# Kernel tuning notes

Measured on AMD Instinct MI355X. Metric: run time of the kernel, lower is better.

## Reference

```python
import jax, jax.numpy as jnp
import numpy as np

K = 5               # kernel size of the causal/dilated convs
N_LAYERS = 30       # params.n_dilation_conv_layers
CYCLE = 10          # n_dilation_conv_layers / n_dilation_cycles
MU = 255.0          # quantization_channels - 1 for mu-law expansion
B, T = 8, 262144


def dil_causal_conv(x, w, b, d):
    """Single-channel dilated causal conv. x:[B,1,T], w:[K], b:scalar/[1]."""
    P = (K - 1) * d
    xp = jnp.pad(x, ((0, 0), (0, 0), (P, 0)))
    Tn = x.shape[-1]
    # cross-correlation, matching torch Conv1d with left pad then right crop
    y = w[0] * xp[..., 0:Tn]
    for j in range(1, K):
        y = y + w[j] * xp[..., j * d: j * d + Tn]
    return y + b


def setup_inputs() -> dict:
    key = jax.random.key(0)
    ks = jax.random.split(key, 14)
    n = lambda k, shape, s=0.2: jax.random.normal(k, shape, dtype=jnp.float32) * s
    return {
        "x": jax.random.normal(ks[0], (B, 1, T), dtype=jnp.float32),
        "causal_w": n(ks[1], (K,)),
        "causal_b": n(ks[2], (1,)),
        "filter_w": n(ks[3], (N_LAYERS, K)),
        "filter_b": n(ks[4], (N_LAYERS,)),
        "gate_w": n(ks[5], (N_LAYERS, K)),
        "gate_b": n(ks[6], (N_LAYERS,)),
        "res_w": n(ks[7], (N_LAYERS,)),
        "res_b": n(ks[8], (N_LAYERS,)),
        "conv1_w": n(ks[9], (1,)),
        "conv1_b": n(ks[10], (1,)),
        "conv2_w": n(ks[11], (1,)),
        "conv2_b": n(ks[12], (1,)),
    }


def reference(x, causal_w, causal_b, filter_w, filter_b, gate_w, gate_b,
              res_w, res_b, conv1_w, conv1_b, conv2_w, conv2_b):
    dilations = [2 ** (k % CYCLE) for k in range(N_LAYERS)]
    h = dil_causal_conv(x, causal_w, causal_b, 1)
    skip = jnp.zeros_like(h)
    for k, d in enumerate(dilations):
        f = jnp.tanh(dil_causal_conv(h, filter_w[k], filter_b[k], d))
        g = jax.nn.sigmoid(dil_causal_conv(h, gate_w[k], gate_b[k], d))
        o = f * g                      # gated activation (skip output)
        h = res_w[k] * o + res_b[k] + h  # 1x1 residual conv + residual add
        skip = skip + o
    out = conv1_w * jax.nn.relu(skip) + conv1_b   # 1x1 conv
    out = conv2_w * jax.nn.relu(out) + conv2_b    # 1x1 conv
    # mu-law expanding, quantization_channels=256
    out = jnp.sign(out) * jnp.expm1(jnp.abs(out) * jnp.log1p(MU)) / MU
    return jax.nn.softmax(out, axis=-1)
```

## Files before the change

kernel.cpp:

```cpp
#include <hip/hip_runtime.h>

#define T_LEN 262144
#define B_SZ 8
#define CHUNK 8192
#define HALO 4096
#define NTHREADS 1024
#define NGROUPW 3
#define NGROUPS ((CHUNK + HALO) / 4)
#define CHUNKS_PER_ROW (T_LEN / CHUNK)
#define NBLOCKS (B_SZ * CHUNKS_PER_ROW)
#define LOG2E 1.4426950408889634f
#define NEG2LOG2E (-2.8853900817779268f)
#define NEGLOG2E  (-1.4426950408889634f)

__device__ __forceinline__ float frcp(float x)  { return __builtin_amdgcn_rcpf(x); }
__device__ __forceinline__ float fexp2(float x) { return __builtin_amdgcn_exp2f(x); }
__device__ __forceinline__ float4 ld4(const float* p) { return *(const float4*)p; }
__device__ __forceinline__ void st4(float* p, float4 v) { *(float4*)p = v; }
__device__ __forceinline__ float4 f4(float v) { return make_float4(v, v, v, v); }
__device__ __forceinline__ float4 fma4(float a, float4 b, float4 c) {
    return make_float4(__builtin_fmaf(a, b.x, c.x), __builtin_fmaf(a, b.y, c.y),
                       __builtin_fmaf(a, b.z, c.z), __builtin_fmaf(a, b.w, c.w));
}
__device__ __forceinline__ float4 add4(float4 a, float4 b) {
    return make_float4(a.x + b.x, a.y + b.y, a.z + b.z, a.w + b.w);
}
__device__ __forceinline__ float gate1(float af, float ag) {
    float E1 = fexp2(af), E2 = fexp2(ag);
    float d1 = 1.0f + E1;
    float den = __builtin_fmaf(E2, d1, d1);
    return (1.0f - E1) * frcp(den);
}
__device__ __forceinline__ float4 resid4(float rwv, float4 o, float4 hw, float rbv) {
    return make_float4(__builtin_fmaf(rwv, o.x, hw.x + rbv), __builtin_fmaf(rwv, o.y, hw.y + rbv),
                       __builtin_fmaf(rwv, o.z, hw.z + rbv), __builtin_fmaf(rwv, o.w, hw.w + rbv));
}
__device__ __forceinline__ float mulaw(float v, float c1wv, float c1bv, float c2wv, float c2bv) {
    float a  = __builtin_fmaf(c1wv, fmaxf(v, 0.0f), c1bv);
    float b2 = __builtin_fmaf(c2wv, fmaxf(a, 0.0f), c2bv);
    float m  = fexp2(fabsf(b2) * 8.0f) - 1.0f;
    return copysignf(m * (1.0f / 255.0f), b2);
}
__device__ __forceinline__ uint2 pk4(float4 v) {
    uint2 u;
    u.x = (__float_as_uint(v.y) & 0xffff0000u) | (__float_as_uint(v.x) >> 16);
    u.y = (__float_as_uint(v.w) & 0xffff0000u) | (__float_as_uint(v.z) >> 16);
    return u;
}
__device__ __forceinline__ float4 up4(uint2 u) {
    return make_float4(__uint_as_float(u.x << 16), __uint_as_float(u.x),
                       __uint_as_float(u.y << 16), __uint_as_float(u.y));
}

template <int STAGE>
__global__ __launch_bounds__(NTHREADS, 4)
void stage_kernel(const float* __restrict__ in,
                  const float* __restrict__ cw, const float* __restrict__ cb,
                  const float* __restrict__ fw, const float* __restrict__ fb,
                  const float* __restrict__ gw, const float* __restrict__ gb,
                  const float* __restrict__ rw, const float* __restrict__ rb,
                  float* __restrict__ hout, float* __restrict__ skio,
                  const float* __restrict__ c1w, const float* __restrict__ c1b,
                  const float* __restrict__ c2w, const float* __restrict__ c2b,
                  float2* __restrict__ blockstats)
{
    __shared__ uint2 bufl[2][NGROUPS];
    __shared__ float red[NTHREADS / 64];

    const int tid = threadIdx.x;
    const int bid = blockIdx.x;
    const int row = bid / CHUNKS_PER_ROW;
    const int chunk = bid % CHUNKS_PER_ROW;
    const int rowbase = row * T_LEN;
    const int base_t = chunk * CHUNK;
    const bool first = (chunk == 0);
    const float* inb = in + rowbase + base_t - HALO;

    float4 h[NGROUPW];
    #pragma unroll
    for (int w = 0; w < NGROUPW; ++w) {
        int G = tid + w * NTHREADS;
        if (w == 0 && first) h[w] = f4(0.0f);
        else                 h[w] = ld4(inb + 4 * G);
        bufl[0][G] = pk4(h[w]);
    }
    float4 sk1, sk2;
    if (STAGE == 0) { sk1 = f4(0.0f); sk2 = f4(0.0f); }
    else {
        sk1 = ld4(skio + rowbase + base_t + 4 * tid);
        sk2 = ld4(skio + rowbase + base_t + 4096 + 4 * tid);
    }
    __syncthreads();

    int c = 0;
    if (STAGE == 0) {
        const float c0 = cw[4], c1 = cw[3], c2 = cw[2], c3 = cw[1], c4 = cw[0];
        const float bb = cb[0];
        #pragma unroll
        for (int w = 0; w < NGROUPW; ++w) {
            int G = tid + w * NTHREADS;
            int gm = G - 1; if (w == 0) gm = gm < 0 ? 0 : gm;
            float4 T = up4(bufl[0][gm]);
            float4 hw = h[w];
            float4 t1 = make_float4(T.w, hw.x, hw.y, hw.z);
            float4 t2 = make_float4(T.z, T.w, hw.x, hw.y);
            float4 t3 = make_float4(T.y, T.z, T.w, hw.x);
            float4 t4 = make_float4(T.x, T.y, T.z, T.w);
            float4 acc = fma4(c0, hw, f4(bb));
            acc = fma4(c1, t1, acc);
            acc = fma4(c2, t2, acc);
            acc = fma4(c3, t3, acc);
            acc = fma4(c4, t4, acc);
            if (w == 0 && first) acc = f4(0.0f);
            h[w] = acc;
            bufl[1][G] = pk4(acc);
        }
        __syncthreads();
        c = 1;
    }

    #pragma unroll
    for (int k = 0; k < 10; ++k) {
        const int d = 1 << k;
        const int L = STAGE * 10 + k;
        const float* fwL = fw + 5 * L;
        const float* gwL = gw + 5 * L;
        const float wf0 = fwL[4] * NEG2LOG2E, wf1 = fwL[3] * NEG2LOG2E,
                    wf2 = fwL[2] * NEG2LOG2E, wf3 = fwL[1] * NEG2LOG2E,
                    wf4 = fwL[0] * NEG2LOG2E;
        const float wg0 = gwL[4] * NEGLOG2E, wg1 = gwL[3] * NEGLOG2E,
                    wg2 = gwL[2] * NEGLOG2E, wg3 = gwL[1] * NEGLOG2E,
                    wg4 = gwL[0] * NEGLOG2E;
        const float fbv = fb[L] * NEG2LOG2E, gbv = gb[L] * NEGLOG2E;
        const float rwv = rw[L], rbv = rb[L];

        #pragma unroll
        for (int w = 0; w < NGROUPW; ++w) {
            const int G = tid + w * NTHREADS;
            float4 hw = h[w];
            float4 t1, t2, t3, t4;
            if (d >= 4) {
                const int DG = d >> 2;
                int g1 = G - DG, g2 = G - 2 * DG, g3 = G - 3 * DG, g4 = G - 4 * DG;
                if (w == 0) {
                    g1 = g1 < 0 ? 0 : g1; g2 = g2 < 0 ? 0 : g2;
                    g3 = g3 < 0 ? 0 : g3; g4 = g4 < 0 ? 0 : g4;
                }
                t1 = up4(bufl[c][g1]);
                t2 = up4(bufl[c][g2]);
                t3 = up4(bufl[c][g3]);
                t4 = up4(bufl[c][g4]);
            } else if (d == 1) {
                int gm = G - 1; if (w == 0) gm = gm < 0 ? 0 : gm;
                float4 T = up4(bufl[c][gm]);
                t1 = make_float4(T.w, hw.x, hw.y, hw.z);
                t2 = make_float4(T.z, T.w, hw.x, hw.y);
                t3 = make_float4(T.y, T.z, T.w, hw.x);
                t4 = make_float4(T.x, T.y, T.z, T.w);
            } else {
                int gm1 = G - 1, gm2 = G - 2;
                if (w == 0) { gm1 = gm1 < 0 ? 0 : gm1; gm2 = gm2 < 0 ? 0 : gm2; }
                float4 T1 = up4(bufl[c][gm1]);
                float4 T2 = up4(bufl[c][gm2]);
                t1 = make_float4(T1.z, T1.w, hw.x, hw.y);
                t2 = T1;
                t3 = make_float4(T2.z, T2.w, T1.x, T1.y);
                t4 = T2;
            }
            float4 af = fma4(wf0, hw, f4(fbv));
            af = fma4(wf1, t1, af); af = fma4(wf2, t2, af);
            af = fma4(wf3, t3, af); af = fma4(wf4, t4, af);
            float4 ag = fma4(wg0, hw, f4(gbv));
            ag = fma4(wg1, t1, ag); ag = fma4(wg2, t2, ag);
            ag = fma4(wg3, t3, ag); ag = fma4(wg4, t4, ag);
            float4 o;
            o.x = gate1(af.x, ag.x);
            o.y = gate1(af.y, ag.y);
            o.z = gate1(af.z, ag.z);
            o.w = gate1(af.w, ag.w);
            float4 nh = resid4(rwv, o, hw, rbv);
            if (w == 0 && first) nh = f4(0.0f);
            h[w] = nh;
            if (k < 9) bufl[c ^ 1][G] = pk4(nh);
            if (w == 1) sk1 = add4(sk1, o);
            if (w == 2) sk2 = add4(sk2, o);
        }
        if (k < 9) __syncthreads();
        c ^= 1;
    }

    if (STAGE < 2) {
        st4(hout + rowbase + base_t + 4 * tid, h[1]);
        st4(hout + rowbase + base_t + 4096 + 4 * tid, h[2]);
        st4(skio + rowbase + base_t + 4 * tid, sk1);
        st4(skio + rowbase + base_t + 4096 + 4 * tid, sk2);
    } else {
        const float c1wv = c1w[0], c1bv = c1b[0], c2wv = c2w[0], c2bv = c2b[0];
        float4 p1, p2;
        p1.x = mulaw(sk1.x, c1wv, c1bv, c2wv, c2bv);
        p1.y = mulaw(sk1.y, c1wv, c1bv, c2wv, c2bv);
        p1.z = mulaw(sk1.z, c1wv, c1bv, c2wv, c2bv);
        p1.w = mulaw(sk1.w, c1wv, c1bv, c2wv, c2bv);
        p2.x = mulaw(sk2.x, c1wv, c1bv, c2wv, c2bv);
        p2.y = mulaw(sk2.y, c1wv, c1bv, c2wv, c2bv);
        p2.z = mulaw(sk2.z, c1wv, c1bv, c2wv, c2bv);
        p2.w = mulaw(sk2.w, c1wv, c1bv, c2wv, c2bv);
        st4(skio + rowbase + base_t + 4 * tid, p1);
        st4(skio + rowbase + base_t + 4096 + 4 * tid, p2);

        float pmax = fmaxf(fmaxf(fmaxf(p1.x, p1.y), fmaxf(p1.z, p1.w)),
                           fmaxf(fmaxf(p2.x, p2.y), fmaxf(p2.z, p2.w)));
        #pragma unroll
        for (int off = 32; off; off >>= 1) pmax = fmaxf(pmax, __shfl_xor(pmax, off, 64));
        if ((tid & 63) == 0) red[tid >> 6] = pmax;
        __syncthreads();
        float bmax = red[0];
        #pragma unroll
        for (int i = 1; i < NTHREADS / 64; ++i) bmax = fmaxf(bmax, red[i]);
        __syncthreads();

        float ps = fexp2((p1.x - bmax) * LOG2E) + fexp2((p1.y - bmax) * LOG2E)
                 + fexp2((p1.z - bmax) * LOG2E) + fexp2((p1.w - bmax) * LOG2E)
                 + fexp2((p2.x - bmax) * LOG2E) + fexp2((p2.y - bmax) * LOG2E)
                 + fexp2((p2.z - bmax) * LOG2E) + fexp2((p2.w - bmax) * LOG2E);
        #pragma unroll
        for (int off = 32; off; off >>= 1) ps += __shfl_xor(ps, off, 64);
        if ((tid & 63) == 0) red[tid >> 6] = ps;
        __syncthreads();
        if (tid == 0) {
            float s = 0.0f;
            #pragma unroll
            for (int i = 0; i < NTHREADS / 64; ++i) s += red[i];
            blockstats[bid] = make_float2(bmax, s);
        }
    }
}

__global__ __launch_bounds__(64)
void combine_kernel(const float2* __restrict__ bs, float2* __restrict__ rs)
{
    const int row = blockIdx.x;
    const int lane = threadIdx.x;
    float bm = -3.0e38f, s = 0.0f;
    if (lane < CHUNKS_PER_ROW) {
        float2 v = bs[row * CHUNKS_PER_ROW + lane];
        bm = v.x; s = v.y;
    }
    float m = bm;
    #pragma unroll
    for (int off = 32; off; off >>= 1) m = fmaxf(m, __shfl_xor(m, off, 64));
    float c = s * fexp2((bm - m) * LOG2E);
    #pragma unroll
    for (int off = 32; off; off >>= 1) c += __shfl_xor(c, off, 64);
    if (lane == 0) rs[row] = make_float2(m, 1.0f / c);
}

__global__ __launch_bounds__(NTHREADS)
void norm_kernel(float* __restrict__ p, const float2* __restrict__ rs)
{
    const int tid = threadIdx.x, bid = blockIdx.x;
    const int row = bid / CHUNKS_PER_ROW;
    const float2 st = rs[row];
    const int base = row * T_LEN + (bid % CHUNKS_PER_ROW) * CHUNK + 4 * tid;
    #pragma unroll
    for (int part = 0; part < 2; ++part) {
        float* q = p + base + part * 4096;
        float4 v = ld4(q);
        v.x = fexp2((v.x - st.x) * LOG2E) * st.y;
        v.y = fexp2((v.y - st.x) * LOG2E) * st.y;
        v.z = fexp2((v.z - st.x) * LOG2E) * st.y;
        v.w = fexp2((v.w - st.x) * LOG2E) * st.y;
        st4(q, v);
    }
}

extern "C" void kernel_launch(void* const* d_in, const int* in_sizes, int n_in,
                              void* d_out, int out_size, void* d_ws, size_t ws_size,
                              hipStream_t stream)
{
    (void)in_sizes; (void)n_in; (void)out_size; (void)ws_size;
    const float* x   = (const float*)d_in[0];
    const float* cw  = (const float*)d_in[1];
    const float* cb  = (const float*)d_in[2];
    const float* fw  = (const float*)d_in[3];
    const float* fb  = (const float*)d_in[4];
    const float* gw  = (const float*)d_in[5];
    const float* gb  = (const float*)d_in[6];
    const float* rw  = (const float*)d_in[7];
    const float* rb  = (const float*)d_in[8];
    const float* c1w = (const float*)d_in[9];
    const float* c1b = (const float*)d_in[10];
    const float* c2w = (const float*)d_in[11];
    const float* c2b = (const float*)d_in[12];
    float* out = (float*)d_out;

    const size_t NTOT = (size_t)B_SZ * T_LEN;
    float*  hA = (float*)d_ws;
    float*  hB = (float*)((char*)d_ws + NTOT * 4);
    float2* bs = (float2*)((char*)d_ws + 2 * NTOT * 4);
    float2* rs = (float2*)((char*)d_ws + 2 * NTOT * 4 + 4096);

    stage_kernel<0><<<NBLOCKS, NTHREADS, 0, stream>>>(x,  cw, cb, fw, fb, gw, gb, rw, rb,
                                                      hA, out, c1w, c1b, c2w, c2b, bs);
    stage_kernel<1><<<NBLOCKS, NTHREADS, 0, stream>>>(hA, cw, cb, fw, fb, gw, gb, rw, rb,
                                                      hB, out, c1w, c1b, c2w, c2b, bs);
    stage_kernel<2><<<NBLOCKS, NTHREADS, 0, stream>>>(hB, cw, cb, fw, fb, gw, gb, rw, rb,
                                                      nullptr, out, c1w, c1b, c2w, c2b, bs);
    combine_kernel<<<B_SZ, 64, 0, stream>>>(bs, rs);
    norm_kernel<<<NBLOCKS, NTHREADS, 0, stream>>>(out, rs);
}
```

Baseline: 85.04 us.

## Halve chunk size, store inter-stage activations as bf16, skip dead halo work

Shrinks each block's output chunk from 8192 to 4096 samples while keeping the 4096-sample halo. Each thread now holds two float4 groups instead of three, and occupancy is raised to 8 blocks per CU. Inter-stage hidden states are written and read as packed bf16 (uint2) to halve that global traffic. Halo positions whose results cannot reach the output are skipped per layer, and those paths drop the clamp logic. The cost is double the blocks, so halo recompute rises relative to useful work, bf16 truncation is added between stages, and the combine kernel now assumes exactly 64 chunks per row.

```diff
diff --git a/kernel.cpp b/kernel.cpp
--- a/kernel.cpp
+++ b/kernel.cpp
@@ -2,10 +2,9 @@
 
 #define T_LEN 262144
 #define B_SZ 8
-#define CHUNK 8192
+#define CHUNK 4096
 #define HALO 4096
 #define NTHREADS 1024
-#define NGROUPW 3
 #define NGROUPS ((CHUNK + HALO) / 4)
 #define CHUNKS_PER_ROW (T_LEN / CHUNK)
 #define NBLOCKS (B_SZ * CHUNKS_PER_ROW)
@@ -13,27 +12,39 @@
 #define NEG2LOG2E (-2.8853900817779268f)
 #define NEGLOG2E  (-1.4426950408889634f)
 
+typedef float f32x4 __attribute__((ext_vector_type(4)));
+
 __device__ __forceinline__ float frcp(float x)  { return __builtin_amdgcn_rcpf(x); }
 __device__ __forceinline__ float fexp2(float x) { return __builtin_amdgcn_exp2f(x); }
-__device__ __forceinline__ float4 ld4(const float* p) { return *(const float4*)p; }
-__device__ __forceinline__ void st4(float* p, float4 v) { *(float4*)p = v; }
-__device__ __forceinline__ float4 f4(float v) { return make_float4(v, v, v, v); }
-__device__ __forceinline__ float4 fma4(float a, float4 b, float4 c) {
-    return make_float4(__builtin_fmaf(a, b.x, c.x), __builtin_fmaf(a, b.y, c.y),
-                       __builtin_fmaf(a, b.z, c.z), __builtin_fmaf(a, b.w, c.w));
-}
-__device__ __forceinline__ float4 add4(float4 a, float4 b) {
-    return make_float4(a.x + b.x, a.y + b.y, a.z + b.z, a.w + b.w);
-}
-__device__ __forceinline__ float gate1(float af, float ag) {
-    float E1 = fexp2(af), E2 = fexp2(ag);
-    float d1 = 1.0f + E1;
-    float den = __builtin_fmaf(E2, d1, d1);
-    return (1.0f - E1) * frcp(den);
-}
-__device__ __forceinline__ float4 resid4(float rwv, float4 o, float4 hw, float rbv) {
-    return make_float4(__builtin_fmaf(rwv, o.x, hw.x + rbv), __builtin_fmaf(rwv, o.y, hw.y + rbv),
-                       __builtin_fmaf(rwv, o.z, hw.z + rbv), __builtin_fmaf(rwv, o.w, hw.w + rbv));
+__device__ __forceinline__ f32x4 splat(float s) { f32x4 r = {s, s, s, s}; return r; }
+__device__ __forceinline__ f32x4 sfma(float s, f32x4 v, f32x4 a) {
+    return __builtin_elementwise_fma(splat(s), v, a);
+}
+__device__ __forceinline__ uint2 pk4(f32x4 v) {
+    uint2 u;
+    u.x = __builtin_amdgcn_perm(__float_as_uint(v.y), __float_as_uint(v.x), 0x07060302u);
+    u.y = __builtin_amdgcn_perm(__float_as_uint(v.w), __float_as_uint(v.z), 0x07060302u);
+    return u;
+}
+__device__ __forceinline__ f32x4 up4(uint2 u) {
+    f32x4 r;
+    r.x = __uint_as_float(u.x << 16);
+    r.y = __uint_as_float(u.x);
+    r.z = __uint_as_float(u.y << 16);
+    r.w = __uint_as_float(u.y);
+    return r;
+}
+__device__ __forceinline__ f32x4 gate4(f32x4 af, f32x4 ag) {
+    f32x4 E1, E2;
+    E1.x = fexp2(af.x); E1.y = fexp2(af.y); E1.z = fexp2(af.z); E1.w = fexp2(af.w);
+    E2.x = fexp2(ag.x); E2.y = fexp2(ag.y); E2.z = fexp2(ag.z); E2.w = fexp2(ag.w);
+    f32x4 d1  = E1 + splat(1.0f);
+    f32x4 den = __builtin_elementwise_fma(E2, d1, d1);
+    f32x4 num = splat(1.0f) - E1;
+    f32x4 r;
+    r.x = num.x * frcp(den.x); r.y = num.y * frcp(den.y);
+    r.z = num.z * frcp(den.z); r.w = num.w * frcp(den.w);
+    return r;
 }
 __device__ __forceinline__ float mulaw(float v, float c1wv, float c1bv, float c2wv, float c2bv) {
     float a  = __builtin_fmaf(c1wv, fmaxf(v, 0.0f), c1bv);
@@ -41,25 +52,15 @@
     float m  = fexp2(fabsf(b2) * 8.0f) - 1.0f;
     return copysignf(m * (1.0f / 255.0f), b2);
 }
-__device__ __forceinline__ uint2 pk4(float4 v) {
-    uint2 u;
-    u.x = (__float_as_uint(v.y) & 0xffff0000u) | (__float_as_uint(v.x) >> 16);
-    u.y = (__float_as_uint(v.w) & 0xffff0000u) | (__float_as_uint(v.z) >> 16);
-    return u;
-}
-__device__ __forceinline__ float4 up4(uint2 u) {
-    return make_float4(__uint_as_float(u.x << 16), __uint_as_float(u.x),
-                       __uint_as_float(u.y << 16), __uint_as_float(u.y));
-}
 
 template <int STAGE>
-__global__ __launch_bounds__(NTHREADS, 4)
-void stage_kernel(const float* __restrict__ in,
+__global__ __launch_bounds__(NTHREADS, 8)
+void stage_kernel(const void* __restrict__ in_,
                   const float* __restrict__ cw, const float* __restrict__ cb,
                   const float* __restrict__ fw, const float* __restrict__ fb,
                   const float* __restrict__ gw, const float* __restrict__ gb,
                   const float* __restrict__ rw, const float* __restrict__ rb,
-                  float* __restrict__ hout, float* __restrict__ skio,
+                  uint2* __restrict__ hout, float* __restrict__ skio,
                   const float* __restrict__ c1w, const float* __restrict__ c1b,
                   const float* __restrict__ c2w, const float* __restrict__ c2b,
                   float2* __restrict__ blockstats)
@@ -74,22 +75,30 @@
     const int rowbase = row * T_LEN;
     const int base_t = chunk * CHUNK;
     const bool first = (chunk == 0);
-    const float* inb = in + rowbase + base_t - HALO;
-
-    float4 h[NGROUPW];
-    #pragma unroll
-    for (int w = 0; w < NGROUPW; ++w) {
-        int G = tid + w * NTHREADS;
-        if (w == 0 && first) h[w] = f4(0.0f);
-        else                 h[w] = ld4(inb + 4 * G);
-        bufl[0][G] = pk4(h[w]);
-    }
-    float4 sk1, sk2;
-    if (STAGE == 0) { sk1 = f4(0.0f); sk2 = f4(0.0f); }
-    else {
-        sk1 = ld4(skio + rowbase + base_t + 4 * tid);
-        sk2 = ld4(skio + rowbase + base_t + 4096 + 4 * tid);
-    }
+
+    f32x4 h[2];
+    if (STAGE == 0) {
+        const float* inb = (const float*)in_ + rowbase + base_t - HALO;
+        #pragma unroll
+        for (int w = 0; w < 2; ++w) {
+            int G = tid + w * NTHREADS;
+            if (w == 0 && first) h[w] = splat(0.0f);
+            else                 h[w] = *(const f32x4*)(inb + 4 * G);
+            bufl[0][G] = pk4(h[w]);
+        }
+    } else {
+        const uint2* inb = (const uint2*)in_ + ((rowbase + base_t - HALO) >> 2);
+        #pragma unroll
+        for (int w = 0; w < 2; ++w) {
+            int G = tid + w * NTHREADS;
+            uint2 u = (w == 0 && first) ? make_uint2(0u, 0u) : inb[G];
+            bufl[0][G] = u;
+            h[w] = up4(u);
+        }
+    }
+    f32x4 sk;
+    if (STAGE == 0) sk = splat(0.0f);
+    else            sk = *(const f32x4*)(skio + rowbase + base_t + 4 * tid);
     __syncthreads();
 
     int c = 0;
@@ -97,21 +106,20 @@
         const float c0 = cw[4], c1 = cw[3], c2 = cw[2], c3 = cw[1], c4 = cw[0];
         const float bb = cb[0];
         #pragma unroll
-        for (int w = 0; w < NGROUPW; ++w) {
+        for (int w = 0; w < 2; ++w) {
             int G = tid + w * NTHREADS;
             int gm = G - 1; if (w == 0) gm = gm < 0 ? 0 : gm;
-            float4 T = up4(bufl[0][gm]);
-            float4 hw = h[w];
-            float4 t1 = make_float4(T.w, hw.x, hw.y, hw.z);
-            float4 t2 = make_float4(T.z, T.w, hw.x, hw.y);
-            float4 t3 = make_float4(T.y, T.z, T.w, hw.x);
-            float4 t4 = make_float4(T.x, T.y, T.z, T.w);
-            float4 acc = fma4(c0, hw, f4(bb));
-            acc = fma4(c1, t1, acc);
-            acc = fma4(c2, t2, acc);
-            acc = fma4(c3, t3, acc);
-            acc = fma4(c4, t4, acc);
-            if (w == 0 && first) acc = f4(0.0f);
+            f32x4 T = up4(bufl[0][gm]);
+            f32x4 hw = h[w];
+            f32x4 t1 = __builtin_shufflevector(T, hw, 3, 4, 5, 6);
+            f32x4 t2 = __builtin_shufflevector(T, hw, 2, 3, 4, 5);
+            f32x4 t3 = __builtin_shufflevector(T, hw, 1, 2, 3, 4);
+            f32x4 acc = sfma(c0, hw, splat(bb));
+            acc = sfma(c1, t1, acc);
+            acc = sfma(c2, t2, acc);
+            acc = sfma(c3, t3, acc);
+            acc = sfma(c4, T, acc);
+            if (w == 0 && first) acc = splat(0.0f);
             h[w] = acc;
             bufl[1][G] = pk4(acc);
         }
@@ -135,81 +143,62 @@
         const float rwv = rw[L], rbv = rb[L];
 
         #pragma unroll
-        for (int w = 0; w < NGROUPW; ++w) {
+        for (int w = 0; w < 2; ++w) {
+            if (w == 0 && k == 9) continue;
             const int G = tid + w * NTHREADS;
-            float4 hw = h[w];
-            float4 t1, t2, t3, t4;
+            if (w == 0 && tid < (2 << k)) continue;
+            f32x4 hw = h[w];
+            f32x4 t1, t2, t3, t4;
             if (d >= 4) {
                 const int DG = d >> 2;
-                int g1 = G - DG, g2 = G - 2 * DG, g3 = G - 3 * DG, g4 = G - 4 * DG;
-                if (w == 0) {
-                    g1 = g1 < 0 ? 0 : g1; g2 = g2 < 0 ? 0 : g2;
-                    g3 = g3 < 0 ? 0 : g3; g4 = g4 < 0 ? 0 : g4;
-                }
-                t1 = up4(bufl[c][g1]);
-                t2 = up4(bufl[c][g2]);
-                t3 = up4(bufl[c][g3]);
-                t4 = up4(bufl[c][g4]);
+                t1 = up4(bufl[c][G - DG]);
+                t2 = up4(bufl[c][G - 2 * DG]);
+                t3 = up4(bufl[c][G - 3 * DG]);
+                t4 = up4(bufl[c][G - 4 * DG]);
             } else if (d == 1) {
-                int gm = G - 1; if (w == 0) gm = gm < 0 ? 0 : gm;
-                float4 T = up4(bufl[c][gm]);
-                t1 = make_float4(T.w, hw.x, hw.y, hw.z);
-                t2 = make_float4(T.z, T.w, hw.x, hw.y);
-                t3 = make_float4(T.y, T.z, T.w, hw.x);
-                t4 = make_float4(T.x, T.y, T.z, T.w);
+                f32x4 T = up4(bufl[c][G - 1]);
+                t1 = __builtin_shufflevector(T, hw, 3, 4, 5, 6);
+                t2 = __builtin_shufflevector(T, hw, 2, 3, 4, 5);
+                t3 = __builtin_shufflevector(T, hw, 1, 2, 3, 4);
+                t4 = T;
             } else {
-                int gm1 = G - 1, gm2 = G - 2;
-                if (w == 0) { gm1 = gm1 < 0 ? 0 : gm1; gm2 = gm2 < 0 ? 0 : gm2; }
-                float4 T1 = up4(bufl[c][gm1]);
-                float4 T2 = up4(bufl[c][gm2]);
-                t1 = make_float4(T1.z, T1.w, hw.x, hw.y);
+                f32x4 T1 = up4(bufl[c][G - 1]);
+                f32x4 T2 = up4(bufl[c][G - 2]);
+                t1 = __builtin_shufflevector(T1, hw, 2, 3, 4, 5);
                 t2 = T1;
-                t3 = make_float4(T2.z, T2.w, T1.x, T1.y);
+                t3 = __builtin_shufflevector(T2, T1, 2, 3, 4, 5);
                 t4 = T2;
             }
-            float4 af = fma4(wf0, hw, f4(fbv));
-            af = fma4(wf1, t1, af); af = fma4(wf2, t2, af);
-            af = fma4(wf3, t3, af); af = fma4(wf4, t4, af);
-            float4 ag = fma4(wg0, hw, f4(gbv));
-            ag = fma4(wg1, t1, ag); ag = fma4(wg2, t2, ag);
-            ag = fma4(wg3, t3, ag); ag = fma4(wg4, t4, ag);
-            float4 o;
-            o.x = gate1(af.x, ag.x);
-            o.y = gate1(af.y, ag.y);
-            o.z = gate1(af.z, ag.z);
-            o.w = gate1(af.w, ag.w);
-            float4 nh = resid4(rwv, o, hw, rbv);
-            if (w == 0 && first) nh = f4(0.0f);
+            f32x4 af = sfma(wf0, hw, splat(fbv));
+            af = sfma(wf1, t1, af); af = sfma(wf2, t2, af);
+            af = sfma(wf3, t3, af); af = sfma(wf4, t4, af);
+            f32x4 ag = sfma(wg0, hw, splat(gbv));
+            ag = sfma(wg1, t1, ag); ag = sfma(wg2, t2, ag);
+            ag = sfma(wg3, t3, ag); ag = sfma(wg4, t4, ag);
+            f32x4 o = gate4(af, ag);
+            f32x4 nh = sfma(rwv, o, hw + splat(rbv));
+            if (w == 0 && first) nh = splat(0.0f);
             h[w] = nh;
             if (k < 9) bufl[c ^ 1][G] = pk4(nh);
-            if (w == 1) sk1 = add4(sk1, o);
-            if (w == 2) sk2 = add4(sk2, o);
+            if (w == 1) sk += o;
         }
         if (k < 9) __syncthreads();
         c ^= 1;
     }
 
     if (STAGE < 2) {
-        st4(hout + rowbase + base_t + 4 * tid, h[1]);
-        st4(hout + rowbase + base_t + 4096 + 4 * tid, h[2]);
-        st4(skio + rowbase + base_t + 4 * tid, sk1);
-        st4(skio + rowbase + base_t + 4096 + 4 * tid, sk2);
+        hout[((rowbase + base_t) >> 2) + tid] = pk4(h[1]);
+        *(f32x4*)(skio + rowbase + base_t + 4 * tid) = sk;
     } else {
         const float c1wv = c1w[0], c1bv = c1b[0], c2wv = c2w[0], c2bv = c2b[0];
-        float4 p1, p2;
-        p1.x = mulaw(sk1.x, c1wv, c1bv, c2wv, c2bv);
-        p1.y = mulaw(sk1.y, c1wv, c1bv, c2wv, c2bv);
-        p1.z = mulaw(sk1.z, c1wv, c1bv, c2wv, c2bv);
-        p1.w = mulaw(sk1.w, c1wv, c1bv, c2wv, c2bv);
-        p2.x = mulaw(sk2.x, c1wv, c1bv, c2wv, c2bv);
-        p2.y = mulaw(sk2.y, c1wv, c1bv, c2wv, c2bv);
-        p2.z = mulaw(sk2.z, c1wv, c1bv, c2wv, c2bv);
-        p2.w = mulaw(sk2.w, c1wv, c1bv, c2wv, c2bv);
-        st4(skio + rowbase + base_t + 4 * tid, p1);
-        st4(skio + rowbase + base_t + 4096 + 4 * tid, p2);
-
-        float pmax = fmaxf(fmaxf(fmaxf(p1.x, p1.y), fmaxf(p1.z, p1.w)),
-                           fmaxf(fmaxf(p2.x, p2.y), fmaxf(p2.z, p2.w)));
+        f32x4 p;
+        p.x = mulaw(sk.x, c1wv, c1bv, c2wv, c2bv);
+        p.y = mulaw(sk.y, c1wv, c1bv, c2wv, c2bv);
+        p.z = mulaw(sk.z, c1wv, c1bv, c2wv, c2bv);
+        p.w = mulaw(sk.w, c1wv, c1bv, c2wv, c2bv);
+        *(f32x4*)(skio + rowbase + base_t + 4 * tid) = p;
+
+        float pmax = fmaxf(fmaxf(p.x, p.y), fmaxf(p.z, p.w));
         #pragma unroll
         for (int off = 32; off; off >>= 1) pmax = fmaxf(pmax, __shfl_xor(pmax, off, 64));
         if ((tid & 63) == 0) red[tid >> 6] = pmax;
@@ -219,10 +208,8 @@
         for (int i = 1; i < NTHREADS / 64; ++i) bmax = fmaxf(bmax, red[i]);
         __syncthreads();
 
-        float ps = fexp2((p1.x - bmax) * LOG2E) + fexp2((p1.y - bmax) * LOG2E)
-                 + fexp2((p1.z - bmax) * LOG2E) + fexp2((p1.w - bmax) * LOG2E)
-                 + fexp2((p2.x - bmax) * LOG2E) + fexp2((p2.y - bmax) * LOG2E)
-                 + fexp2((p2.z - bmax) * LOG2E) + fexp2((p2.w - bmax) * LOG2E);
+        float ps = fexp2((p.x - bmax) * LOG2E) + fexp2((p.y - bmax) * LOG2E)
+                 + fexp2((p.z - bmax) * LOG2E) + fexp2((p.w - bmax) * LOG2E);
         #pragma unroll
         for (int off = 32; off; off >>= 1) ps += __shfl_xor(ps, off, 64);
         if ((tid & 63) == 0) red[tid >> 6] = ps;
@@ -241,18 +228,15 @@
 {
     const int row = blockIdx.x;
     const int lane = threadIdx.x;
-    float bm = -3.0e38f, s = 0.0f;
-    if (lane < CHUNKS_PER_ROW) {
-        float2 v = bs[row * CHUNKS_PER_ROW + lane];
-        bm = v.x; s = v.y;
-    }
+    float2 v = bs[row * CHUNKS_PER_ROW + lane];
+    float bm = v.x, s = v.y;
     float m = bm;
     #pragma unroll
     for (int off = 32; off; off >>= 1) m = fmaxf(m, __shfl_xor(m, off, 64));
-    float c = s * fexp2((bm - m) * LOG2E);
+    float cc = s * fexp2((bm - m) * LOG2E);
     #pragma unroll
-    for (int off = 32; off; off >>= 1) c += __shfl_xor(c, off, 64);
-    if (lane == 0) rs[row] = make_float2(m, 1.0f / c);
+    for (int off = 32; off; off >>= 1) cc += __shfl_xor(cc, off, 64);
+    if (lane == 0) rs[row] = make_float2(m, 1.0f / cc);
 }
 
 __global__ __launch_bounds__(NTHREADS)
@@ -261,17 +245,13 @@
     const int tid = threadIdx.x, bid = blockIdx.x;
     const int row = bid / CHUNKS_PER_ROW;
     const float2 st = rs[row];
-    const int base = row * T_LEN + (bid % CHUNKS_PER_ROW) * CHUNK + 4 * tid;
-    #pragma unroll
-    for (int part = 0; part < 2; ++part) {
-        float* q = p + base + part * 4096;
-        float4 v = ld4(q);
-        v.x = fexp2((v.x - st.x) * LOG2E) * st.y;
-        v.y = fexp2((v.y - st.x) * LOG2E) * st.y;
-        v.z = fexp2((v.z - st.x) * LOG2E) * st.y;
-        v.w = fexp2((v.w - st.x) * LOG2E) * st.y;
-        st4(q, v);
-    }
+    float* q = p + row * T_LEN + (bid % CHUNKS_PER_ROW) * CHUNK + 4 * tid;
+    f32x4 v = *(const f32x4*)q;
+    v.x = fexp2((v.x - st.x) * LOG2E) * st.y;
+    v.y = fexp2((v.y - st.x) * LOG2E) * st.y;
+    v.z = fexp2((v.z - st.x) * LOG2E) * st.y;
+    v.w = fexp2((v.w - st.x) * LOG2E) * st.y;
+    *(f32x4*)q = v;
 }
 
 extern "C" void kernel_launch(void* const* d_in, const int* in_sizes, int n_in,
@@ -295,10 +275,10 @@
     float* out = (float*)d_out;
 
     const size_t NTOT = (size_t)B_SZ * T_LEN;
-    float*  hA = (float*)d_ws;
-    float*  hB = (float*)((char*)d_ws + NTOT * 4);
-    float2* bs = (float2*)((char*)d_ws + 2 * NTOT * 4);
-    float2* rs = (float2*)((char*)d_ws + 2 * NTOT * 4 + 4096);
+    uint2*  hA = (uint2*)d_ws;
+    uint2*  hB = (uint2*)((char*)d_ws + NTOT * 2);
+    float2* bs = (float2*)((char*)d_ws + NTOT * 4);
+    float2* rs = (float2*)((char*)d_ws + NTOT * 4 + 8192);
 
     stage_kernel<0><<<NBLOCKS, NTHREADS, 0, stream>>>(x,  cw, cb, fw, fb, gw, gb, rw, rb,
                                                       hA, out, c1w, c1b, c2w, c2b, bs);
```

New measurement: 129.9 us. 1.53x slower.
